# Optimization experiments

Measured on AMD Instinct MI355X. Metric: run time of the kernel, lower is better.

## Reference

```python
import jax, jax.numpy as jnp
import numpy as np
import math

V, E, R, B, T, L = 32000, 256, 1024, 64, 2048, 3
EPS = 1e-5


def setup_inputs() -> dict:
    key = jax.random.key(0)
    ks = jax.random.split(key, 8)
    x = jax.random.randint(ks[0], (B, T), 0, V)
    embed_w = jax.random.normal(ks[1], (V, E), jnp.float32)
    Win0 = jax.random.normal(ks[2], (E, R), jnp.float32) / math.sqrt(E) / 0.9
    Win1 = jax.random.normal(ks[3], (R, R), jnp.float32) / math.sqrt(R) / 0.9
    Win2 = jax.random.normal(ks[4], (R, R), jnp.float32) / math.sqrt(R) / 0.9
    R0 = jax.random.normal(ks[5], (R, R), jnp.float32) / math.sqrt(R) / 0.9
    R1 = jax.random.normal(ks[6], (R, R), jnp.float32) / math.sqrt(R) / 0.9
    R2 = jax.random.normal(ks[7], (R, R), jnp.float32) / math.sqrt(R) / 0.9
    ln_w = jnp.ones((R,), jnp.float32)
    ln_b = jnp.zeros((R,), jnp.float32)
    return dict(x=x, embed_w=embed_w, Win0=Win0, Win1=Win1, Win2=Win2,
                R0=R0, R1=R1, R2=R2, ln_w=ln_w, ln_b=ln_b)


def reference(x, embed_w, Win0, Win1, Win2, R0, R1, R2, ln_w, ln_b):
    Wins = (Win0, Win1, Win2)
    Rs = (R0, R1, R2)
    x_embed = embed_w[x]                        # [B, T, E]
    b = x.shape[0]
    rsz = R0.shape[0]
    init = tuple(jnp.zeros((b, rsz), x_embed.dtype) for _ in range(L))

    def step(states, xt):                       # xt: [B, E]
        cur = xt
        new = []
        for i in range(L):                      # 'deep': layer i>0 consumes states[i-1] (fresh)
            s = jnp.tanh(states[i] @ Rs[i] + cur @ Wins[i])
            new.append(s)
            cur = s
        return tuple(new), None

    states, _ = jax.lax.scan(step, init, jnp.swapaxes(x_embed, 0, 1))  # scan over T
    h = states[-1]                              # [B, R]
    mu = jnp.mean(h, axis=-1, keepdims=True)
    var = jnp.var(h, axis=-1, keepdims=True)
    return (h - mu) / jnp.sqrt(var + EPS) * ln_w + ln_b
```

## Files before the change

### kernel.cpp

```cpp
#include <hip/hip_runtime.h>

#define VV    32000
#define EE    256
#define RSZ   1024
#define BB    64
#define TT    2048
#define NGRP  3
#define EPSLN 1e-5f

#define NBLK_PER_GRP 64
#define NBLK  (NBLK_PER_GRP * NGRP)
#define NTHR  512
#define SLAB  (BB * RSZ)

#define BAR_OFF (NGRP * 2 * SLAB)

__device__ __forceinline__ void fma_step8x4(const float4 (&b)[8], const float* wrow,
                                            float (&acc)[8][4]) {
#pragma unroll
    for (int j = 0; j < 4; ++j) {
        const float4 w = *reinterpret_cast<const float4*>(wrow + j * 16);
#pragma unroll
        for (int r = 0; r < 8; ++r) {
            const float a = reinterpret_cast<const float*>(&b[r])[j];
            acc[r][0] = fmaf(a, w.x, acc[r][0]);
            acc[r][1] = fmaf(a, w.y, acc[r][1]);
            acc[r][2] = fmaf(a, w.z, acc[r][2]);
            acc[r][3] = fmaf(a, w.w, acc[r][3]);
        }
    }
}

__device__ __forceinline__ void ld8(float4 (&b)[8], const float* const (&p)[8],
                                    int off) {
#pragma unroll
    for (int r = 0; r < 8; ++r)
        b[r] = *reinterpret_cast<const float4*>(p[r] + off);
}

template<int NSTEPS>
__device__ __forceinline__ void dot8(const float* const (&p)[8],
                                     const float* w, float (&acc)[8][4]) {
    float4 A[8], B[8];
    ld8(A, p, 0);
    ld8(B, p, 4);
    for (int j = 0; j < NSTEPS - 2; j += 2) {
        fma_step8x4(A, w + j * 64, acc);
        ld8(A, p, (j + 2) * 4);
        fma_step8x4(B, w + (j + 1) * 64, acc);
        ld8(B, p, (j + 3) * 4);
    }
    fma_step8x4(A, w + (NSTEPS - 2) * 64, acc);
    fma_step8x4(B, w + (NSTEPS - 1) * 64, acc);
}

__global__ __launch_bounds__(NTHR, 1)
void reservoir_main(const int*   __restrict__ x,
                    const float* __restrict__ embed_w,
                    const float* __restrict__ Win0,
                    const float* __restrict__ Win1,
                    const float* __restrict__ Win2,
                    const float* __restrict__ Rm0,
                    const float* __restrict__ Rm1,
                    const float* __restrict__ Rm2,
                    const float* __restrict__ ln_w,
                    const float* __restrict__ ln_b,
                    float*       __restrict__ states,
                    unsigned*    __restrict__ bar,
                    float*       __restrict__ out)
{
    const int blk   = blockIdx.x;
    const int grp   = blk >> 6;
    const int gb    = blk & 63;
    const int c0    = gb << 4;
    const int tid   = threadIdx.x;
    const int kg    = tid >> 5;
    const int idx   = tid & 31;
    const int rbase = (idx >> 2) << 3;
    const int cg4   = (idx & 3) << 2;
    const int ph    = rbase >> 4;

    const float* Wl  = (grp == 0) ? Win0 : ((grp == 1) ? Win1 : Win2);
    const float* Rl  = (grp == 0) ? Rm0  : ((grp == 1) ? Rm1  : Rm2);
    const int    Kw  = (grp == 0) ? EE : RSZ;
    const int    KwS = Kw >> 4;

    __shared__ float wlds[2048 * 16];
    __shared__ float pbuf[16][16][20];

    for (int i = tid; i < RSZ * 16; i += NTHR) {
        const int k = i >> 4, c = i & 15;
        wlds[i] = Rl[(size_t)k * RSZ + c0 + c];
    }
    for (int i = tid; i < Kw * 16; i += NTHR) {
        const int k = i >> 4, c = i & 15;
        wlds[RSZ * 16 + i] = Wl[(size_t)k * RSZ + c0 + c];
    }
    __syncthreads();

    unsigned* leaf  = bar;
    unsigned* root  = bar + 128;
    unsigned* epoch = bar + 160;

    float* const sl = states + (size_t)grp * 2 * SLAB;
    const float* const wRb = wlds + (kg << 6) * 16 + cg4;
    const float* const wWb = wlds + (RSZ + kg * KwS) * 16 + cg4;

    int xidx[8];
    if (grp == 0) {
#pragma unroll
        for (int r = 0; r < 8; ++r) xidx[r] = x[(rbase + r) * TT + 0];
    }

    for (int tick = 0; tick < TT + NGRP - 1; ++tick) {
        const int t = tick - grp;
        if (0 <= t && t < TT) {
            const float* sprev = sl + (size_t)((t + 1) & 1) * SLAB;

            float acc[8][4];
#pragma unroll
            for (int r = 0; r < 8; ++r)
#pragma unroll
                for (int c = 0; c < 4; ++c) acc[r][c] = 0.f;

            {
                const float* aR[8];
#pragma unroll
                for (int r = 0; r < 8; ++r)
                    aR[r] = sprev + (size_t)(rbase + r) * RSZ + (kg << 6);
                dot8<16>(aR, wRb, acc);
            }
            {
                const float* aW[8];
                if (grp == 0) {
#pragma unroll
                    for (int r = 0; r < 8; ++r)
                        aW[r] = embed_w + (size_t)xidx[r] * EE + kg * KwS;
                    dot8<4>(aW, wWb, acc);
                } else {
                    const float* cb = states + ((size_t)(grp - 1) * 2 + (t & 1)) * SLAB;
#pragma unroll
                    for (int r = 0; r < 8; ++r)
                        aW[r] = cb + (size_t)(rbase + r) * RSZ + kg * KwS;
                    dot8<16>(aW, wWb, acc);
                }
            }

            if (grp == 0 && t + 1 < TT) {
#pragma unroll
                for (int r = 0; r < 8; ++r) xidx[r] = x[(rbase + r) * TT + t + 1];
            }

            float* sout = sl + (size_t)(t & 1) * SLAB;
#pragma unroll
            for (int p = 0; p < 4; ++p) {
                if (ph == p) {
#pragma unroll
                    for (int r = 0; r < 8; ++r) {
                        const int lr = (rbase + r) & 15;
                        *reinterpret_cast<float4*>(
                            &pbuf[kg][lr][cg4 ^ ((lr & 3) << 2)])
                            = make_float4(acc[r][0], acc[r][1], acc[r][2], acc[r][3]);
                    }
                }
                __syncthreads();
                if (tid < 256) {
                    const int rl = tid >> 4, col = tid & 15;
                    const int cw = ((col & 12) ^ ((rl & 3) << 2)) | (col & 3);
                    float s = 0.f;
#pragma unroll
                    for (int g = 0; g < 16; ++g) s += pbuf[g][rl][cw];
                    sout[(size_t)(16 * p + rl) * RSZ + c0 + col] = tanhf(s);
                }
                __syncthreads();
            }
        }

        __syncthreads();
        if (tid == 0) {
            __threadfence();
            const unsigned target = (unsigned)(tick + 1);
            unsigned prev = atomicAdd(&leaf[(blk & 7) << 4], 1u);
            if (prev == 24u * target - 1u) {
                prev = atomicAdd(root, 1u);
                if (prev == 8u * target - 1u)
                    __hip_atomic_store(epoch, target, __ATOMIC_RELEASE,
                                       __HIP_MEMORY_SCOPE_AGENT);
            }
            while (__hip_atomic_load(epoch, __ATOMIC_RELAXED,
                                     __HIP_MEMORY_SCOPE_AGENT) < target)
                __builtin_amdgcn_s_sleep(2);
            __threadfence();
        }
        __syncthreads();
    }

    if (blk < BB) {
        const float* h = states + ((size_t)2 * 2 + 1) * SLAB + (size_t)blk * RSZ;
        float* red = &pbuf[0][0][0];

        const float hv0 = h[tid];
        const float hv1 = h[tid + 512];
        float v = hv0 + hv1;
#pragma unroll
        for (int o = 32; o > 0; o >>= 1) v += __shfl_down(v, o, 64);
        if ((tid & 63) == 0) red[tid >> 6] = v;
        __syncthreads();
        if (tid == 0) {
            float s = 0.f;
#pragma unroll
            for (int i = 0; i < 8; ++i) s += red[i];
            red[20] = s / (float)RSZ;
        }
        __syncthreads();
        const float mu = red[20];
        const float d0 = hv0 - mu, d1 = hv1 - mu;
        v = d0 * d0 + d1 * d1;
#pragma unroll
        for (int o = 32; o > 0; o >>= 1) v += __shfl_down(v, o, 64);
        __syncthreads();
        if ((tid & 63) == 0) red[tid >> 6] = v;
        __syncthreads();
        if (tid == 0) {
            float s = 0.f;
#pragma unroll
            for (int i = 0; i < 8; ++i) s += red[i];
            red[21] = rsqrtf(s / (float)RSZ + EPSLN);
        }
        __syncthreads();
        const float inv = red[21];
        out[blk * RSZ + tid]       = d0 * inv * ln_w[tid]       + ln_b[tid];
        out[blk * RSZ + tid + 512] = d1 * inv * ln_w[tid + 512] + ln_b[tid + 512];
    }
}

extern "C" void kernel_launch(void* const* d_in, const int* in_sizes, int n_in,
                              void* d_out, int out_size, void* d_ws, size_t ws_size,
                              hipStream_t stream) {
    const int*   x       = (const int*)  d_in[0];
    const float* embed_w = (const float*)d_in[1];
    const float* Win0    = (const float*)d_in[2];
    const float* Win1    = (const float*)d_in[3];
    const float* Win2    = (const float*)d_in[4];
    const float* Rm0     = (const float*)d_in[5];
    const float* Rm1     = (const float*)d_in[6];
    const float* Rm2     = (const float*)d_in[7];
    const float* ln_w    = (const float*)d_in[8];
    const float* ln_b    = (const float*)d_in[9];
    float*       out     = (float*)d_out;
    float*       states  = (float*)d_ws;
    unsigned*    bar     = (unsigned*)((float*)d_ws + BAR_OFF);

    hipMemsetAsync(d_ws, 0, (size_t)BAR_OFF * sizeof(float) + 4096, stream);

    void* args[] = {
        (void*)&x, (void*)&embed_w,
        (void*)&Win0, (void*)&Win1, (void*)&Win2,
        (void*)&Rm0, (void*)&Rm1, (void*)&Rm2,
        (void*)&ln_w, (void*)&ln_b,
        (void*)&states, (void*)&bar, (void*)&out
    };
    hipLaunchCooperativeKernel(reinterpret_cast<void*>(reservoir_main),
                               dim3(NBLK), dim3(NTHR), args, 0, stream);
}
```

Measured before the change: 63.82 ms.

## Replace global tree barrier with per-group dataflow counters

```diff
diff --git a/kernel.cpp b/kernel.cpp
--- a/kernel.cpp
+++ b/kernel.cpp
@@ -52,6 +52,11 @@
     }
     fma_step8x4(A, w + (NSTEPS - 2) * 64, acc);
     fma_step8x4(B, w + (NSTEPS - 1) * 64, acc);
+}
+
+__device__ __forceinline__ void wait_ge(unsigned* p, unsigned thr) {
+    while (__hip_atomic_load(p, __ATOMIC_RELAXED, __HIP_MEMORY_SCOPE_AGENT) < thr)
+        __builtin_amdgcn_s_sleep(2);
 }
 
 __global__ __launch_bounds__(NTHR, 1)
@@ -98,9 +103,12 @@
     }
     __syncthreads();
 
-    unsigned* leaf  = bar;
-    unsigned* root  = bar + 128;
-    unsigned* epoch = bar + 160;
+    unsigned* done0 = bar;
+    unsigned* done1 = bar + 64;
+    unsigned* done2 = bar + 128;
+    unsigned* doneG = (grp == 0) ? done0 : ((grp == 1) ? done1 : done2);
+    unsigned* doneP = (grp == 0) ? (unsigned*)0 : ((grp == 1) ? done0 : done1);
+    unsigned* doneC = (grp == 0) ? done1 : ((grp == 1) ? done2 : (unsigned*)0);
 
     float* const sl = states + (size_t)grp * 2 * SLAB;
     const float* const wRb = wlds + (kg << 6) * 16 + cg4;
@@ -112,90 +120,91 @@
         for (int r = 0; r < 8; ++r) xidx[r] = x[(rbase + r) * TT + 0];
     }
 
-    for (int tick = 0; tick < TT + NGRP - 1; ++tick) {
-        const int t = tick - grp;
-        if (0 <= t && t < TT) {
-            const float* sprev = sl + (size_t)((t + 1) & 1) * SLAB;
-
-            float acc[8][4];
+    for (int t = 0; t < TT; ++t) {
+        if (tid == 0) {
+            const unsigned ut = (unsigned)t;
+            if (ut)      wait_ge(doneG, 64u * ut);
+            if (doneP)   wait_ge(doneP, 64u * (ut + 1u));
+            if (doneC && t >= 2) wait_ge(doneC, 64u * (ut - 1u));
+            __threadfence();
+        }
+        __syncthreads();
+
+        const float* sprev = sl + (size_t)((t + 1) & 1) * SLAB;
+
+        float acc[8][4];
+#pragma unroll
+        for (int r = 0; r < 8; ++r)
+#pragma unroll
+            for (int c = 0; c < 4; ++c) acc[r][c] = 0.f;
+
+        {
+            const float* aR[8];
 #pragma unroll
             for (int r = 0; r < 8; ++r)
-#pragma unroll
-                for (int c = 0; c < 4; ++c) acc[r][c] = 0.f;
-
-            {
-                const float* aR[8];
+                aR[r] = sprev + (size_t)(rbase + r) * RSZ + (kg << 6);
+            dot8<16>(aR, wRb, acc);
+        }
+        {
+            const float* aW[8];
+            if (grp == 0) {
 #pragma unroll
                 for (int r = 0; r < 8; ++r)
-                    aR[r] = sprev + (size_t)(rbase + r) * RSZ + (kg << 6);
-                dot8<16>(aR, wRb, acc);
+                    aW[r] = embed_w + (size_t)xidx[r] * EE + kg * KwS;
+                dot8<4>(aW, wWb, acc);
+            } else {
+                const float* cb = states + ((size_t)(grp - 1) * 2 + (t & 1)) * SLAB;
+#pragma unroll
+                for (int r = 0; r < 8; ++r)
+                    aW[r] = cb + (size_t)(rbase + r) * RSZ + kg * KwS;
+                dot8<16>(aW, wWb, acc);
             }
-            {
-                const float* aW[8];
-                if (grp == 0) {
-#pragma unroll
-                    for (int r = 0; r < 8; ++r)
-                        aW[r] = embed_w + (size_t)xidx[r] * EE + kg * KwS;
-                    dot8<4>(aW, wWb, acc);
-                } else {
-                    const float* cb = states + ((size_t)(grp - 1) * 2 + (t & 1)) * SLAB;
-#pragma unroll
-                    for (int r = 0; r < 8; ++r)
-                        aW[r] = cb + (size_t)(rbase + r) * RSZ + kg * KwS;
-                    dot8<16>(aW, wWb, acc);
+        }
+
+        if (grp == 0 && t + 1 < TT) {
+#pragma unroll
+            for (int r = 0; r < 8; ++r) xidx[r] = x[(rbase + r) * TT + t + 1];
+        }
+
+        float* sout = sl + (size_t)(t & 1) * SLAB;
+#pragma unroll
+        for (int p = 0; p < 4; ++p) {
+            if (ph == p) {
+#pragma unroll
+                for (int r = 0; r < 8; ++r) {
+                    const int lr = (rbase + r) & 15;
+                    *reinterpret_cast<float4*>(
+                        &pbuf[kg][lr][cg4 ^ ((lr & 3) << 2)])
+                        = make_float4(acc[r][0], acc[r][1], acc[r][2], acc[r][3]);
                 }
             }
-
-            if (grp == 0 && t + 1 < TT) {
-#pragma unroll
-                for (int r = 0; r < 8; ++r) xidx[r] = x[(rbase + r) * TT + t + 1];
+            __syncthreads();
+            if (tid < 256) {
+                const int rl = tid >> 4, col = tid & 15;
+                const int cw = ((col & 12) ^ ((rl & 3) << 2)) | (col & 3);
+                float s = 0.f;
+#pragma unroll
+                for (int g = 0; g < 16; ++g) s += pbuf[g][rl][cw];
+                sout[(size_t)(16 * p + rl) * RSZ + c0 + col] = tanhf(s);
             }
-
-            float* sout = sl + (size_t)(t & 1) * SLAB;
-#pragma unroll
-            for (int p = 0; p < 4; ++p) {
-                if (ph == p) {
-#pragma unroll
-                    for (int r = 0; r < 8; ++r) {
-                        const int lr = (rbase + r) & 15;
-                        *reinterpret_cast<float4*>(
-                            &pbuf[kg][lr][cg4 ^ ((lr & 3) << 2)])
-                            = make_float4(acc[r][0], acc[r][1], acc[r][2], acc[r][3]);
-                    }
-                }
-                __syncthreads();
-                if (tid < 256) {
-                    const int rl = tid >> 4, col = tid & 15;
-                    const int cw = ((col & 12) ^ ((rl & 3) << 2)) | (col & 3);
-                    float s = 0.f;
-#pragma unroll
-                    for (int g = 0; g < 16; ++g) s += pbuf[g][rl][cw];
-                    sout[(size_t)(16 * p + rl) * RSZ + c0 + col] = tanhf(s);
-                }
-                __syncthreads();
-            }
-        }
-
-        __syncthreads();
+            __syncthreads();
+        }
+
         if (tid == 0) {
             __threadfence();
-            const unsigned target = (unsigned)(tick + 1);
-            unsigned prev = atomicAdd(&leaf[(blk & 7) << 4], 1u);
-            if (prev == 24u * target - 1u) {
-                prev = atomicAdd(root, 1u);
-                if (prev == 8u * target - 1u)
-                    __hip_atomic_store(epoch, target, __ATOMIC_RELEASE,
-                                       __HIP_MEMORY_SCOPE_AGENT);
-            }
-            while (__hip_atomic_load(epoch, __ATOMIC_RELAXED,
-                                     __HIP_MEMORY_SCOPE_AGENT) < target)
-                __builtin_amdgcn_s_sleep(2);
+            __hip_atomic_fetch_add(doneG, 1u, __ATOMIC_RELAXED,
+                                   __HIP_MEMORY_SCOPE_AGENT);
+        }
+        __syncthreads();
+    }
+
+    if (blk < BB) {
+        if (tid == 0) {
+            wait_ge(done2, 64u * (unsigned)TT);
             __threadfence();
         }
         __syncthreads();
-    }
-
-    if (blk < BB) {
+
         const float* h = states + ((size_t)2 * 2 + 1) * SLAB + (size_t)blk * RSZ;
         float* red = &pbuf[0][0][0];
 
```

Result: slower. 74.18 ms (+16.2%).

## Stage embedding rows into workspace a tick ahead and halve LDS reduction passes

Applied to the files above, without the earlier changes.

```diff
diff --git a/kernel.cpp b/kernel.cpp
--- a/kernel.cpp
+++ b/kernel.cpp
@@ -14,6 +14,7 @@
 #define SLAB  (BB * RSZ)
 
 #define BAR_OFF (NGRP * 2 * SLAB)
+#define EMB_OFF (BAR_OFF + 1024)
 
 __device__ __forceinline__ void fma_step8x4(const float4 (&b)[8], const float* wrow,
                                             float (&acc)[8][4]) {
@@ -67,6 +68,7 @@
                     const float* __restrict__ ln_b,
                     float*       __restrict__ states,
                     unsigned*    __restrict__ bar,
+                    float*       __restrict__ estage,
                     float*       __restrict__ out)
 {
     const int blk   = blockIdx.x;
@@ -78,7 +80,8 @@
     const int idx   = tid & 31;
     const int rbase = (idx >> 2) << 3;
     const int cg4   = (idx & 3) << 2;
-    const int ph    = rbase >> 4;
+    const int lane  = tid & 63;
+    const int g2    = tid >> 6;
 
     const float* Wl  = (grp == 0) ? Win0 : ((grp == 1) ? Win1 : Win2);
     const float* Rl  = (grp == 0) ? Rm0  : ((grp == 1) ? Rm1  : Rm2);
@@ -86,7 +89,7 @@
     const int    KwS = Kw >> 4;
 
     __shared__ float wlds[2048 * 16];
-    __shared__ float pbuf[16][16][20];
+    __shared__ float pbuf[8][32][20];
 
     for (int i = tid; i < RSZ * 16; i += NTHR) {
         const int k = i >> 4, c = i & 15;
@@ -106,13 +109,7 @@
     const float* const wRb = wlds + (kg << 6) * 16 + cg4;
     const float* const wWb = wlds + (RSZ + kg * KwS) * 16 + cg4;
 
-    int xidx[8];
-    if (grp == 0) {
-#pragma unroll
-        for (int r = 0; r < 8; ++r) xidx[r] = x[(rbase + r) * TT + 0];
-    }
-
-    for (int tick = 0; tick < TT + NGRP - 1; ++tick) {
+    for (int tick = -1; tick < TT + NGRP - 1; ++tick) {
         const int t = tick - grp;
         if (0 <= t && t < TT) {
             const float* sprev = sl + (size_t)((t + 1) & 1) * SLAB;
@@ -133,9 +130,10 @@
             {
                 const float* aW[8];
                 if (grp == 0) {
+                    const float* eb = estage + (size_t)(t & 1) * (BB * EE);
 #pragma unroll
                     for (int r = 0; r < 8; ++r)
-                        aW[r] = embed_w + (size_t)xidx[r] * EE + kg * KwS;
+                        aW[r] = eb + (rbase + r) * EE + kg * KwS;
                     dot8<4>(aW, wWb, acc);
                 } else {
                     const float* cb = states + ((size_t)(grp - 1) * 2 + (t & 1)) * SLAB;
@@ -146,40 +144,51 @@
                 }
             }
 
-            if (grp == 0 && t + 1 < TT) {
-#pragma unroll
-                for (int r = 0; r < 8; ++r) xidx[r] = x[(rbase + r) * TT + t + 1];
-            }
+#pragma unroll
+            for (int r = 0; r < 8; ++r)
+#pragma unroll
+                for (int c = 0; c < 4; ++c)
+                    acc[r][c] += __shfl_down(acc[r][c], 32, 64);
 
             float* sout = sl + (size_t)(t & 1) * SLAB;
 #pragma unroll
-            for (int p = 0; p < 4; ++p) {
-                if (ph == p) {
+            for (int p = 0; p < 2; ++p) {
+                if (lane < 32 && (lane >> 4) == p) {
 #pragma unroll
                     for (int r = 0; r < 8; ++r) {
-                        const int lr = (rbase + r) & 15;
+                        const int lr = (rbase + r) & 31;
                         *reinterpret_cast<float4*>(
-                            &pbuf[kg][lr][cg4 ^ ((lr & 3) << 2)])
+                            &pbuf[g2][lr][cg4 ^ ((lr & 3) << 2)])
                             = make_float4(acc[r][0], acc[r][1], acc[r][2], acc[r][3]);
                     }
                 }
                 __syncthreads();
-                if (tid < 256) {
+                {
                     const int rl = tid >> 4, col = tid & 15;
                     const int cw = ((col & 12) ^ ((rl & 3) << 2)) | (col & 3);
                     float s = 0.f;
 #pragma unroll
-                    for (int g = 0; g < 16; ++g) s += pbuf[g][rl][cw];
-                    sout[(size_t)(16 * p + rl) * RSZ + c0 + col] = tanhf(s);
+                    for (int g = 0; g < 8; ++g) s += pbuf[g][rl][cw];
+                    sout[(size_t)(32 * p + rl) * RSZ + c0 + col] = tanhf(s);
                 }
                 __syncthreads();
             }
         }
 
+        if (grp == 0 && tick + 1 < TT) {
+            if (tid < 64) {
+                const int tok = x[gb * TT + (tick + 1)];
+                const float4 v = *reinterpret_cast<const float4*>(
+                    embed_w + (size_t)tok * EE + (tid << 2));
+                *reinterpret_cast<float4*>(
+                    estage + (size_t)((tick + 1) & 1) * (BB * EE) + gb * EE + (tid << 2)) = v;
+            }
+        }
+
         __syncthreads();
         if (tid == 0) {
             __threadfence();
-            const unsigned target = (unsigned)(tick + 1);
+            const unsigned target = (unsigned)(tick + 2);
             unsigned prev = atomicAdd(&leaf[(blk & 7) << 4], 1u);
             if (prev == 24u * target - 1u) {
                 prev = atomicAdd(root, 1u);
@@ -250,6 +259,7 @@
     float*       out     = (float*)d_out;
     float*       states  = (float*)d_ws;
     unsigned*    bar     = (unsigned*)((float*)d_ws + BAR_OFF);
+    float*       estage  = (float*)d_ws + EMB_OFF;
 
     hipMemsetAsync(d_ws, 0, (size_t)BAR_OFF * sizeof(float) + 4096, stream);
 
@@ -258,7 +268,7 @@
         (void*)&Win0, (void*)&Win1, (void*)&Win2,
         (void*)&Rm0, (void*)&Rm1, (void*)&Rm2,
         (void*)&ln_w, (void*)&ln_b,
-        (void*)&states, (void*)&bar, (void*)&out
+        (void*)&states, (void*)&bar, (void*)&estage, (void*)&out
     };
     hipLaunchCooperativeKernel(reinterpret_cast<void*>(reservoir_main),
                                dim3(NBLK), dim3(NTHR), args, 0, stream);
```

Result: slower. 143.5 ms (+124.9%).
